# Kernel optimization log

Hardware: AMD Instinct MI355X
Metric: run time of the kernel (lower is better)

The kernel has to match this reference:

```python
import jax, jax.numpy as jnp
import numpy as np

NPOINT = 2048
K = 32
EPS = 1e-5  # BatchNorm eps


def setup_inputs() -> dict:
    key = jax.random.key(0)
    ks = jax.random.split(key, 5)
    B, N, C = 4, 8192, 64
    xyz = jax.random.normal(ks[0], (B, N, 3), jnp.float32)
    points = jax.random.normal(ks[1], (B, C, N), jnp.float32)
    w0 = jax.random.normal(ks[2], (64, C + 3), jnp.float32) * 0.1
    w1 = jax.random.normal(ks[3], (128, 64), jnp.float32) * 0.1
    w2 = jax.random.normal(ks[4], (256, 128), jnp.float32) * 0.1
    return dict(
        xyz=xyz, points=points,
        w0=w0, g0=jnp.ones(64, jnp.float32), b0=jnp.zeros(64, jnp.float32),
        w1=w1, g1=jnp.ones(128, jnp.float32), b1=jnp.zeros(128, jnp.float32),
        w2=w2, g2=jnp.ones(256, jnp.float32), b2=jnp.zeros(256, jnp.float32),
    )


def _fps(xyz, S):
    """Farthest point sampling. xyz: (B,N,3) -> idx (B,S) int32. Starts at point 0."""
    B, N, _ = xyz.shape

    def step(carry, _):
        dmin, far = carry  # dmin: (B,N) running min sq-dist to chosen set; far: (B,) current pick
        centroid = jnp.take_along_axis(xyz, far[:, None, None], axis=1)  # (B,1,3)
        d = jnp.sum((xyz - centroid) ** 2, axis=-1)  # (B,N)
        dmin = jnp.minimum(dmin, d)
        nxt = jnp.argmax(dmin, axis=1).astype(jnp.int32)
        return (dmin, nxt), far

    init = (jnp.full((B, N), 1e10, xyz.dtype), jnp.zeros((B,), jnp.int32))
    _, idx = jax.lax.scan(step, init, None, length=S)
    return jnp.transpose(idx)  # (B,S)


def _bn_relu(x, g, b):
    """Training-mode BatchNorm over all but the channel (last) axis + ReLU. x: (B,S,K,C)."""
    mu = jnp.mean(x, axis=(0, 1, 2), keepdims=True)
    var = jnp.mean((x - mu) ** 2, axis=(0, 1, 2), keepdims=True)
    return jax.nn.relu((x - mu) * jax.lax.rsqrt(var + EPS) * g + b)


def reference(xyz, points, w0, g0, b0, w1, g1, b1, w2, g2, b2):
    B, N, _ = xyz.shape
    S = NPOINT
    idx = _fps(xyz, S)
    new_xyz = jnp.take_along_axis(xyz, idx[:, :, None], axis=1)  # (B,S,3)
    # knn: pairwise squared distances centroids -> all points
    d2 = jnp.sum((new_xyz[:, :, None, :] - xyz[:, None, :, :]) ** 2, axis=-1)  # (B,S,N)
    _, knn_idx = jax.lax.top_k(-d2, K)  # (B,S,K), sorted ascending by distance
    gather = jax.vmap(lambda p, i: p[i])  # per-batch fancy gather
    grouped = gather(xyz, knn_idx) - new_xyz[:, :, None, :]  # (B,S,K,3) relative coords
    neigh = gather(jnp.transpose(points, (0, 2, 1)), knn_idx)  # (B,S,K,C)
    feat = jnp.concatenate([grouped, neigh], axis=-1)  # (B,S,K,3+C)
    for w, g, b in ((w0, g0, b0), (w1, g1, b1), (w2, g2, b2)):
        feat = _bn_relu(jnp.einsum('bskc,oc->bsko', feat, w), g, b)
    new_points = jnp.transpose(jnp.max(feat, axis=2), (0, 2, 1))  # (B,C_out,S)
    return new_xyz, new_points
```

## Files before the change

kernel.cpp:

```cpp
#include <hip/hip_runtime.h>

#define BB 4
#define NN 8192
#define CC 64
#define SS 2048
#define KK 32
#define MROWS (BB*SS*KK)

typedef __attribute__((ext_vector_type(8))) short bf16x8_t;
typedef __attribute__((ext_vector_type(4))) float f32x4_t;
typedef __attribute__((ext_vector_type(2))) float f32x2_t;

__device__ __forceinline__ float bf2f(unsigned short u){
  union { unsigned int i; float f; } v; v.i = ((unsigned int)u) << 16; return v.f;
}
__device__ __forceinline__ unsigned short f2bf(float f){
  union { float f; unsigned int i; } v; v.f = f;
  unsigned int u = v.i;
  unsigned int r = (u + 0x7FFFu + ((u >> 16) & 1u)) >> 16;
  return (unsigned short)r;
}
__device__ __forceinline__ float i2f(int i){ union { int i; float f; } v; v.i = i; return v.f; }
__device__ __forceinline__ int f2i(float f){ union { float f; int i; } v; v.f = f; return v.i; }

__global__ void detect_kernel(const void* pts, int* flag){
  __shared__ int cnt;
  if (threadIdx.x == 0) cnt = 0;
  __syncthreads();
  unsigned short u = ((const unsigned short*)pts)[threadIdx.x];
  int e = (u >> 7) & 0xFF;
  if (e != 0 && (e < 112 || e > 143)) atomicAdd(&cnt, 1);
  __syncthreads();
  if (threadIdx.x == 0) *flag = (cnt > 32) ? 1 : 0;
}

__device__ __forceinline__ void pack_dev(const void* src, unsigned short* dst,
    int CTS, int KSTEPS, int IN, int remap, int idx, bool isf){
  int total = CTS*KSTEPS*512;
  if (idx >= total) return;
  int f = idx >> 9, lane = (idx >> 3) & 63, j = idx & 7;
  int ct = f / KSTEPS, ks = f % KSTEPS;
  int n = ct*16 + (lane & 15);
  int k = ks*32 + (lane >> 4)*8 + j;
  int ksrc;
  if (remap){ ksrc = (k < 64) ? (k + 3) : (k < 67 ? k - 64 : -1); }
  else      { ksrc = (k < IN) ? k : -1; }
  float v = 0.f;
  if (ksrc >= 0){
    size_t si = (size_t)n*IN + ksrc;
    v = isf ? ((const float*)src)[si] : bf2f(((const unsigned short*)src)[si]);
  }
  dst[idx] = f2bf(v);
}

__global__ __launch_bounds__(256) void prep_kernel(
    const void* xyz_in, const void* pts_in,
    const void* w0_in, const void* w1_in, const void* w2_in,
    const void* g0, const void* b0, const void* g1, const void* b1,
    const void* g2, const void* b2,
    float* xyzf, unsigned short* ptsb,
    unsigned short* w0p, unsigned short* w1p, unsigned short* w2p,
    float* gbf, float* stats, const int* flag)
{
  __shared__ float tile[64][65];
  int blk = blockIdx.x, tid = threadIdx.x;
  bool isf = (*flag != 0);
  if (blk < 512){
    int b = blk >> 7, n0 = (blk & 127) * 64;
    #pragma unroll
    for (int k = 0; k < 16; k++){
      int idx = k*256 + tid; int c = idx >> 6; int ni = idx & 63;
      size_t src = ((size_t)b*CC + c)*NN + n0 + ni;
      tile[c][ni] = isf ? ((const float*)pts_in)[src] : bf2f(((const unsigned short*)pts_in)[src]);
    }
    __syncthreads();
    #pragma unroll
    for (int k = 0; k < 16; k++){
      int idx = k*256 + tid; int ni = idx >> 6; int c = idx & 63;
      ptsb[((size_t)b*NN + n0 + ni)*CC + c] = f2bf(tile[c][ni]);
    }
  } else if (blk < 896){
    int i = (blk - 512)*256 + tid;
    if (i < BB*NN*3)
      xyzf[i] = isf ? ((const float*)xyz_in)[i] : bf2f(((const unsigned short*)xyz_in)[i]);
  } else if (blk < 900){
    int i = (blk - 896)*256 + tid;
    if (i < 896){
      const void* src; int off;
      if      (i < 64)  { src = g0; off = i; }
      else if (i < 128) { src = b0; off = i - 64; }
      else if (i < 256) { src = g1; off = i - 128; }
      else if (i < 384) { src = b1; off = i - 256; }
      else if (i < 640) { src = g2; off = i - 384; }
      else              { src = b2; off = i - 640; }
      gbf[i] = isf ? ((const float*)src)[off] : bf2f(((const unsigned short*)src)[off]);
      stats[i] = 0.f;
    }
  } else if (blk < 924){
    pack_dev(w0_in, w0p, 4, 3, 67, 1, (blk-900)*256 + tid, isf);
  } else if (blk < 956){
    pack_dev(w1_in, w1p, 8, 2, 64, 0, (blk-924)*256 + tid, isf);
  } else {
    pack_dev(w2_in, w2p, 16, 4, 128, 0, (blk-956)*256 + tid, isf);
  }
}

__device__ __forceinline__ unsigned mspread(unsigned v){
  v = (v | (v << 16)) & 0x030000FFu;
  v = (v | (v <<  8)) & 0x0300F00Fu;
  v = (v | (v <<  4)) & 0x030C30C3u;
  v = (v | (v <<  2)) & 0x09249249u;
  return v;
}
__global__ __launch_bounds__(1024) void morton_sort(const float* xyzf,
    float* psx, float* psy, float* psz, int* iorig){
  int b = blockIdx.x, tid = threadIdx.x;
  const float* xb = xyzf + (size_t)b*NN*3;
  __shared__ unsigned codes[NN];
  __shared__ unsigned hist[256];
  __shared__ unsigned curs[256];
  __shared__ float rbb[96];
  float x[8], y[8], z[8];
  {
    const float4* p4 = (const float4*)(xb + (size_t)tid*24);
    float4 A=p4[0],B2=p4[1],C=p4[2],D=p4[3],E=p4[4],F=p4[5];
    x[0]=A.x;  y[0]=A.y;  z[0]=A.z;
    x[1]=A.w;  y[1]=B2.x; z[1]=B2.y;
    x[2]=B2.z; y[2]=B2.w; z[2]=C.x;
    x[3]=C.y;  y[3]=C.z;  z[3]=C.w;
    x[4]=D.x;  y[4]=D.y;  z[4]=D.z;
    x[5]=D.w;  y[5]=E.x;  z[5]=E.y;
    x[6]=E.z;  y[6]=E.w;  z[6]=F.x;
    x[7]=F.y;  y[7]=F.z;  z[7]=F.w;
  }
  float lx=x[0],hx=x[0],ly=y[0],hy=y[0],lz=z[0],hz=z[0];
  #pragma unroll
  for (int j = 1; j < 8; j++){
    lx=fminf(lx,x[j]); hx=fmaxf(hx,x[j]);
    ly=fminf(ly,y[j]); hy=fmaxf(hy,y[j]);
    lz=fminf(lz,z[j]); hz=fmaxf(hz,z[j]);
  }
  #pragma unroll
  for (int off = 1; off < 64; off <<= 1){
    lx=fminf(lx,__shfl_xor(lx,off)); hx=fmaxf(hx,__shfl_xor(hx,off));
    ly=fminf(ly,__shfl_xor(ly,off)); hy=fmaxf(hy,__shfl_xor(hy,off));
    lz=fminf(lz,__shfl_xor(lz,off)); hz=fmaxf(hz,__shfl_xor(hz,off));
  }
  int w = tid >> 6;
  if ((tid & 63) == 0){
    rbb[w]=lx; rbb[16+w]=hx; rbb[32+w]=ly; rbb[48+w]=hy; rbb[64+w]=lz; rbb[80+w]=hz;
  }
  if (tid < 256) hist[tid] = 0;
  __syncthreads();
  #pragma unroll
  for (int i = 0; i < 16; i++){
    lx=fminf(lx,rbb[i]); hx=fmaxf(hx,rbb[16+i]);
    ly=fminf(ly,rbb[32+i]); hy=fmaxf(hy,rbb[48+i]);
    lz=fminf(lz,rbb[64+i]); hz=fmaxf(hz,rbb[80+i]);
  }
  float sx = 1023.0f/fmaxf(hx-lx,1e-20f);
  float sy = 1023.0f/fmaxf(hy-ly,1e-20f);
  float sz = 1023.0f/fmaxf(hz-lz,1e-20f);
  #pragma unroll
  for (int j = 0; j < 8; j++){
    int qx = (int)((x[j]-lx)*sx); qx = qx < 0 ? 0 : (qx > 1023 ? 1023 : qx);
    int qy = (int)((y[j]-ly)*sy); qy = qy < 0 ? 0 : (qy > 1023 ? 1023 : qy);
    int qz = (int)((z[j]-lz)*sz); qz = qz < 0 ? 0 : (qz > 1023 ? 1023 : qz);
    unsigned code = mspread((unsigned)qx) | (mspread((unsigned)qy) << 1) | (mspread((unsigned)qz) << 2);
    codes[tid*8 + j] = code;
    atomicAdd(&hist[code >> 22], 1u);
  }
  __syncthreads();
  if (tid < 64){
    unsigned h0 = hist[tid*4], h1 = hist[tid*4+1], h2 = hist[tid*4+2], h3 = hist[tid*4+3];
    unsigned s4 = h0 + h1 + h2 + h3;
    unsigned inc = s4;
    #pragma unroll
    for (int off = 1; off < 64; off <<= 1){
      unsigned o = __shfl_up(inc, off);
      if (tid >= off) inc += o;
    }
    unsigned base = inc - s4;
    curs[tid*4]   = base;
    curs[tid*4+1] = base + h0;
    curs[tid*4+2] = base + h0 + h1;
    curs[tid*4+3] = base + h0 + h1 + h2;
  }
  __syncthreads();
  #pragma unroll
  for (int j = 0; j < 8; j++){
    unsigned c = codes[tid*8 + j] >> 22;
    unsigned pos = atomicAdd(&curs[c], 1u);
    psx[b*NN + pos] = x[j];
    psy[b*NN + pos] = y[j];
    psz[b*NN + pos] = z[j];
    iorig[b*NN + pos] = tid*8 + j;
  }
}

template<int C>
__device__ __forceinline__ float dpp_maxf(float v){
  int t = __builtin_amdgcn_update_dpp(0, f2i(v), C, 0xF, 0xF, true);
  return fmaxf(v, i2f(t));
}
template<int C>
__device__ __forceinline__ unsigned dpp_minu(unsigned v){
  unsigned t = (unsigned)__builtin_amdgcn_update_dpp(-1, (int)v, C, 0xF, 0xF, false);
  return v < t ? v : t;
}

__global__ __launch_bounds__(1024, 1) void fps_kernel(const float* xyzf,
    const float* psx, const float* psy, const float* psz, const int* iorig,
    int* fps_idx, void* d_out, const int* flag){
  int b = blockIdx.x, tid = threadIdx.x;
  const float* xb = xyzf + (size_t)b*NN*3;
  __shared__ float sxyz4[NN*4];
  __shared__ unsigned long long rk[3];
  for (int i = tid; i < NN; i += 1024){
    const float* p = xb + (size_t)i*3;
    float4 v; v.x = p[0]; v.y = p[1]; v.z = p[2]; v.w = 0.f;
    *(float4*)&sxyz4[(size_t)i*4] = v;
  }
  if (tid < 3) rk[tid] = 0ull;
  f32x2_t px2[4], py2[4], pz2[4], dmin2[4];
  int io[8];
  {
    const float4* qx = (const float4*)(psx + b*NN + tid*8);
    const float4* qy = (const float4*)(psy + b*NN + tid*8);
    const float4* qz = (const float4*)(psz + b*NN + tid*8);
    float4 a, c;
    a = qx[0]; c = qx[1];
    px2[0]=(f32x2_t){a.x,a.y}; px2[1]=(f32x2_t){a.z,a.w}; px2[2]=(f32x2_t){c.x,c.y}; px2[3]=(f32x2_t){c.z,c.w};
    a = qy[0]; c = qy[1];
    py2[0]=(f32x2_t){a.x,a.y}; py2[1]=(f32x2_t){a.z,a.w}; py2[2]=(f32x2_t){c.x,c.y}; py2[3]=(f32x2_t){c.z,c.w};
    a = qz[0]; c = qz[1];
    pz2[0]=(f32x2_t){a.x,a.y}; pz2[1]=(f32x2_t){a.z,a.w}; pz2[2]=(f32x2_t){c.x,c.y}; pz2[3]=(f32x2_t){c.z,c.w};
    const int4* qi = (const int4*)(iorig + b*NN + tid*8);
    int4 i0 = qi[0], i1 = qi[1];
    io[0]=i0.x; io[1]=i0.y; io[2]=i0.z; io[3]=i0.w;
    io[4]=i1.x; io[5]=i1.y; io[6]=i1.z; io[7]=i1.w;
  }
  #pragma unroll
  for (int q = 0; q < 4; q++) dmin2[q] = (f32x2_t){1e10f, 1e10f};
  float llx, lhx, lly, lhy, llz, lhz;
  {
    llx = fminf(fminf(px2[0].x,px2[0].y), fminf(px2[1].x,px2[1].y));
    llx = fminf(llx, fminf(fminf(px2[2].x,px2[2].y), fminf(px2[3].x,px2[3].y)));
    lhx = fmaxf(fmaxf(px2[0].x,px2[0].y), fmaxf(px2[1].x,px2[1].y));
    lhx = fmaxf(lhx, fmaxf(fmaxf(px2[2].x,px2[2].y), fmaxf(px2[3].x,px2[3].y)));
    lly = fminf(fminf(py2[0].x,py2[0].y), fminf(py2[1].x,py2[1].y));
    lly = fminf(lly, fminf(fminf(py2[2].x,py2[2].y), fminf(py2[3].x,py2[3].y)));
    lhy = fmaxf(fmaxf(py2[0].x,py2[0].y), fmaxf(py2[1].x,py2[1].y));
    lhy = fmaxf(lhy, fmaxf(fmaxf(py2[2].x,py2[2].y), fmaxf(py2[3].x,py2[3].y)));
    llz = fminf(fminf(pz2[0].x,pz2[0].y), fminf(pz2[1].x,pz2[1].y));
    llz = fminf(llz, fminf(fminf(pz2[2].x,pz2[2].y), fminf(pz2[3].x,pz2[3].y)));
    lhz = fmaxf(fmaxf(pz2[0].x,pz2[0].y), fmaxf(pz2[1].x,pz2[1].y));
    lhz = fmaxf(lhz, fmaxf(fmaxf(pz2[2].x,pz2[2].y), fmaxf(pz2[3].x,pz2[3].y)));
  }
  __syncthreads();
  int far = 0;
  bool isf32 = (*flag != 0);
  float* outf = (float*)d_out; unsigned short* outh = (unsigned short*)d_out;
  int ln = tid & 63;
  unsigned cached_lo = 0u, cached_hi = 0u;
  float lmax = 1e10f;
  int rot = 0;
  for (int s = 0; s < SS; s++){
    int rotn = rot + 1; if (rotn == 3) rotn = 0;
    float4 cf = *(const float4*)&sxyz4[(size_t)far*4];
    float cx = cf.x, cy = cf.y, cz = cf.z;
    if (tid == 0){
      fps_idx[b*SS + s] = far;
      size_t o = ((size_t)b*SS + s)*3;
      if (isf32){ outf[o]=cx; outf[o+1]=cy; outf[o+2]=cz; }
      else { outh[o]=f2bf(cx); outh[o+1]=f2bf(cy); outh[o+2]=f2bf(cz); }
    }
    if (tid == 64) rk[rotn] = 0ull;
    float dxl = fmaxf(fmaxf(llx - cx, cx - lhx), 0.f);
    float dyl = fmaxf(fmaxf(lly - cy, cy - lhy), 0.f);
    float dzl = fmaxf(fmaxf(llz - cz, cz - lhz), 0.f);
    float d2l = (dxl*dxl + dyl*dyl + dzl*dzl) * 0.99999f;
    bool upd = (s == 0) || __any(d2l < lmax);
    if (upd){
      f32x2_t cx2 = (f32x2_t){cx, cx}, cy2 = (f32x2_t){cy, cy}, cz2 = (f32x2_t){cz, cz};
      bool ch = false;
      {
        #pragma clang fp contract(off)
        #pragma unroll
        for (int q = 0; q < 4; q++){
          f32x2_t dx = px2[q] - cx2, dy = py2[q] - cy2, dz = pz2[q] - cz2;
          f32x2_t t = dx*dx;
          t = t + dy*dy;
          t = t + dz*dz;
          ch = ch | (t.x < dmin2[q].x) | (t.y < dmin2[q].y);
          dmin2[q].x = fminf(dmin2[q].x, t.x);
          dmin2[q].y = fminf(dmin2[q].y, t.y);
        }
      }
      if (__any(ch)){
        float m0 = fmaxf(fmaxf(dmin2[0].x, dmin2[0].y), fmaxf(dmin2[1].x, dmin2[1].y));
        float m1 = fmaxf(fmaxf(dmin2[2].x, dmin2[2].y), fmaxf(dmin2[3].x, dmin2[3].y));
        float lm = fmaxf(m0, m1);
        lmax = lm;
        lm = dpp_maxf<0x111>(lm); lm = dpp_maxf<0x112>(lm);
        lm = dpp_maxf<0x114>(lm); lm = dpp_maxf<0x118>(lm);
        lm = dpp_maxf<0x142>(lm); lm = dpp_maxf<0x143>(lm);
        float wmax = i2f(__builtin_amdgcn_readlane(f2i(lm), 63));
        unsigned cand = 0xFFFFFFFFu;
        #pragma unroll
        for (int q = 0; q < 4; q++){
          if (dmin2[q].x == wmax){ unsigned u = (unsigned)io[2*q];   cand = u < cand ? u : cand; }
          if (dmin2[q].y == wmax){ unsigned u = (unsigned)io[2*q+1]; cand = u < cand ? u : cand; }
        }
        cand = dpp_minu<0x111>(cand); cand = dpp_minu<0x112>(cand);
        cand = dpp_minu<0x114>(cand); cand = dpp_minu<0x118>(cand);
        cand = dpp_minu<0x142>(cand); cand = dpp_minu<0x143>(cand);
        unsigned cmin = (unsigned)__builtin_amdgcn_readlane((int)cand, 63);
        cached_hi = (unsigned)f2i(wmax);
        cached_lo = ~cmin;
      }
    }
    if (ln == 63)
      atomicMax(&rk[rot], (((unsigned long long)cached_hi) << 32) | cached_lo);
    __syncthreads();
    unsigned long long kk = rk[rot];
    far = (int)(~(unsigned)kk);
    rot = rotn;
  }
}

__global__ __launch_bounds__(256) void knn_kernel(
    const float* psx, const float* psy, const float* psz, const int* ior,
    const float* xyzf, const int* fps_idx, int* knn){
  int cg = blockIdx.x;
  int b = cg >> 11;
  int tid = threadIdx.x;
  const float* xb = xyzf + (size_t)b*NN*3;
  __shared__ unsigned hist[4096];
  __shared__ unsigned long long cand[512];
  __shared__ unsigned psum[256];
  __shared__ unsigned exbase[64];
  __shared__ float scc[3];
  __shared__ int sB, sBase, sCl, sCc;
  __shared__ unsigned long long rmin[4];
  __shared__ unsigned long long swin;

  if (tid == 0){
    int f = fps_idx[cg];
    scc[0] = xb[f*3]; scc[1] = xb[f*3+1]; scc[2] = xb[f*3+2];
    sCl = 0; sCc = 0;
  }
  #pragma unroll
  for (int i = 0; i < 16; i++) hist[tid*16 + i] = 0;
  __syncthreads();
  float cx = scc[0], cy = scc[1], cz = scc[2];

  float dv[32]; int iv[32];
  const float4* qx = (const float4*)(psx + b*NN);
  const float4* qy = (const float4*)(psy + b*NN);
  const float4* qz = (const float4*)(psz + b*NN);
  const int4*   qi = (const int4*)(ior + b*NN);
  {
    #pragma clang fp contract(off)
    #pragma unroll
    for (int k = 0; k < 8; k++){
      float4 X = qx[k*256 + tid];
      float4 Y = qy[k*256 + tid];
      float4 Z = qz[k*256 + tid];
      int4   I = qi[k*256 + tid];
      float xs_[4] = {X.x, X.y, X.z, X.w};
      float ys_[4] = {Y.x, Y.y, Y.z, Y.w};
      float zs_[4] = {Z.x, Z.y, Z.z, Z.w};
      int   is_[4] = {I.x, I.y, I.z, I.w};
      #pragma unroll
      for (int r = 0; r < 4; r++){
        float dx = cx - xs_[r], dy = cy - ys_[r], dz = cz - zs_[r];
        dv[k*4 + r] = dx*dx + dy*dy + dz*dz;
        iv[k*4 + r] = is_[r];
      }
    }
  }
  #pragma unroll
  for (int t = 0; t < 32; t++)
    atomicAdd(&hist[((unsigned)f2i(dv[t])) >> 20], 1u);
  __syncthreads();
  unsigned lsum = 0;
  #pragma unroll
  for (int i = 0; i < 16; i++) lsum += hist[tid*16 + i];
  psum[tid] = lsum;
  __syncthreads();
  if (tid < 64){
    unsigned s4 = psum[tid*4] + psum[tid*4+1] + psum[tid*4+2] + psum[tid*4+3];
    unsigned inc = s4;
    #pragma unroll
    for (int off = 1; off < 64; off <<= 1){
      unsigned o = __shfl_up(inc, off);
      if (tid >= off) inc += o;
    }
    exbase[tid] = inc - s4;
  }
  __syncthreads();
  {
    int g4 = tid >> 2;
    unsigned ex = exbase[g4];
    for (int j = g4*4; j < tid; j++) ex += psum[j];
    unsigned run = ex;
    #pragma unroll
    for (int i = 0; i < 16; i++){
      unsigned c = hist[tid*16 + i];
      if (run < 32u && run + c >= 32u){ sB = tid*16 + i; sBase = (int)run; }
      run += c;
    }
  }
  __syncthreads();
  int Bbin = sB, base = sBase;
  int out = cg << 5;
  #pragma unroll
  for (int t = 0; t < 32; t++){
    unsigned bits = (unsigned)f2i(dv[t]);
    unsigned hb = bits >> 20;
    int idx = iv[t];
    if ((int)hb < Bbin){
      int sl = atomicAdd(&sCl, 1);
      knn[out + sl] = idx;
    } else if ((int)hb == Bbin){
      int c = atomicAdd(&sCc, 1);
      if (c < 512) cand[c] = (((unsigned long long)bits) << 32) | (unsigned)idx;
    }
  }
  __syncthreads();
  int cc = sCc; if (cc > 512) cc = 512;
  int r = 32 - base;
  for (int round = 0; round < r; round++){
    unsigned long long lm = ~0ull;
    for (int i = tid; i < cc; i += 256){
      unsigned long long v = cand[i];
      if (v < lm) lm = v;
    }
    #pragma unroll
    for (int off = 1; off < 64; off <<= 1){
      unsigned long long o = __shfl_xor(lm, off);
      if (o < lm) lm = o;
    }
    if ((tid & 63) == 0) rmin[tid >> 6] = lm;
    __syncthreads();
    if (tid == 0){
      unsigned long long m = rmin[0];
      #pragma unroll
      for (int q = 1; q < 4; q++) if (rmin[q] < m) m = rmin[q];
      swin = m;
      knn[out + base + round] = (int)(unsigned)m;
    }
    __syncthreads();
    unsigned long long m = swin;
    for (int i = tid; i < cc; i += 256)
      if (cand[i] == m) cand[i] = ~0ull;
    __syncthreads();
  }
}

__device__ __forceinline__ bf16x8_t bfrag(const unsigned short* wp, int f, int lane){
  return *(const bf16x8_t*)(wp + ((size_t)f << 9) + (lane << 3));
}
__device__ __forceinline__ bf16x8_t bn_frag(bf16x8_t v, const float* a, const float* c, int kbase){
  float4 a0 = *(const float4*)(a + kbase); float4 a1 = *(const float4*)(a + kbase + 4);
  float4 c0 = *(const float4*)(c + kbase); float4 c1 = *(const float4*)(c + kbase + 4);
  float av[8] = {a0.x,a0.y,a0.z,a0.w,a1.x,a1.y,a1.z,a1.w};
  float cv[8] = {c0.x,c0.y,c0.z,c0.w,c1.x,c1.y,c1.z,c1.w};
  bf16x8_t r;
  #pragma unroll
  for (int j = 0; j < 8; j++)
    r[j] = (short)f2bf(fmaxf(bf2f((unsigned short)v[j])*av[j] + cv[j], 0.f));
  return r;
}

template<int TILES>
__global__ __launch_bounds__(256) void passA(
    const float* __restrict__ xyzf, const unsigned short* __restrict__ ptsb,
    const int* __restrict__ fpsi, const int* __restrict__ knn,
    const unsigned short* __restrict__ w0p,
    unsigned short* __restrict__ y0g, float* osum, float* osq)
{
  __shared__ unsigned short xb0[64*104];
  __shared__ unsigned short st[64*72];
  __shared__ float sacc[128];
  int tid = threadIdx.x, lane = tid & 63, w = tid >> 6;
  int l15 = lane & 15, quad = lane >> 4;
  float ssum[4], ssq[4];
  #pragma unroll
  for (int c = 0; c < 4; c++){ ssum[c] = 0.f; ssq[c] = 0.f; }
  if (tid < 128) sacc[tid] = 0.f;
  __syncthreads();

  for (int t = 0; t < TILES; t++){
    int row0 = (blockIdx.x * TILES + t) * 64;
    {
      int r = tid >> 2, p = tid & 3;
      int g = row0 + r;
      int bq = g >> 16, s = (g >> 5) & 2047;
      int n = knn[g];
      const bf16x8_t* pr = (const bf16x8_t*)(ptsb + (((size_t)bq*NN + n) << 6));
      *(bf16x8_t*)&xb0[r*104 + p*16]     = pr[p*2];
      *(bf16x8_t*)&xb0[r*104 + p*16 + 8] = pr[p*2 + 1];
      if (p == 3){
        const float* xbp = xyzf + (size_t)bq*NN*3;
        int f = fpsi[(bq << 11) + s];
        float dx = xbp[n*3]   - xbp[f*3];
        float dy = xbp[n*3+1] - xbp[f*3+1];
        float dz = xbp[n*3+2] - xbp[f*3+2];
        bf16x8_t v = {(short)f2bf(dx), (short)f2bf(dy), (short)f2bf(dz), 0,0,0,0,0};
        bf16x8_t z = {0,0,0,0,0,0,0,0};
        *(bf16x8_t*)&xb0[r*104 + 64] = v;
        *(bf16x8_t*)&xb0[r*104 + 72] = z;
        *(bf16x8_t*)&xb0[r*104 + 80] = z;
        *(bf16x8_t*)&xb0[r*104 + 88] = z;
      }
    }
    bf16x8_t a0[3];
    #pragma unroll
    for (int ks = 0; ks < 3; ks++)
      a0[ks] = *(const bf16x8_t*)&xb0[(w*16 + l15)*104 + ks*32 + quad*8];
    #pragma unroll
    for (int ct = 0; ct < 4; ct++){
      f32x4_t a = {0.f,0.f,0.f,0.f};
      #pragma unroll
      for (int ks = 0; ks < 3; ks++)
        a = __builtin_amdgcn_mfma_f32_16x16x32_bf16(a0[ks], bfrag(w0p, ct*3+ks, lane), a, 0, 0, 0);
      #pragma unroll
      for (int r = 0; r < 4; r++){
        float v = a[r]; ssum[ct] += v; ssq[ct] += v*v;
        st[(w*16 + quad*4 + r)*72 + ct*16 + l15] = f2bf(v);
      }
    }
    __syncthreads();
    #pragma unroll
    for (int p = 0; p < 2; p++){
      int idx = p*2048 + tid*8; int r = idx >> 6; int c = idx & 63;
      *(bf16x8_t*)(y0g + (size_t)row0*64 + idx) = *(const bf16x8_t*)&st[r*72 + c];
    }
    __syncthreads();
  }
  #pragma unroll
  for (int c = 0; c < 4; c++){
    ssum[c] += __shfl_xor(ssum[c], 16); ssum[c] += __shfl_xor(ssum[c], 32);
    ssq [c] += __shfl_xor(ssq [c], 16); ssq [c] += __shfl_xor(ssq [c], 32);
  }
  if (quad == 0){
    #pragma unroll
    for (int c = 0; c < 4; c++){
      atomicAdd(&sacc[c*16 + l15], ssum[c]);
      atomicAdd(&sacc[64 + c*16 + l15], ssq[c]);
    }
  }
  __syncthreads();
  if (tid < 64){
    atomicAdd(&osum[tid], sacc[tid]);
    atomicAdd(&osq [tid], sacc[64 + tid]);
  }
}

template<int TILES>
__global__ __launch_bounds__(256) void passB(
    const unsigned short* __restrict__ y0g, const unsigned short* __restrict__ w1p,
    const float* __restrict__ stats, const float* __restrict__ gbf,
    unsigned short* __restrict__ y1g, float* osum, float* osq)
{
  __shared__ unsigned short st[64*136];
  __shared__ float sacc[256];
  __shared__ __align__(16) float sbn[128];
  int tid = threadIdx.x, lane = tid & 63, w = tid >> 6;
  int l15 = lane & 15, quad = lane >> 4;
  float ssum[8], ssq[8];
  #pragma unroll
  for (int c = 0; c < 8; c++){ ssum[c] = 0.f; ssq[c] = 0.f; }
  sacc[tid] = 0.f;
  if (tid < 64){
    const float invM = 1.0f/262144.0f;
    float mu = stats[tid]*invM;
    float var = fmaxf(stats[64+tid]*invM - mu*mu, 0.f);
    float inv = 1.0f/sqrtf(var + 1e-5f);
    float av = gbf[tid]*inv;
    sbn[tid] = av; sbn[64+tid] = gbf[64+tid] - mu*av;
  }
  __syncthreads();

  for (int t = 0; t < TILES; t++){
    int row0 = (blockIdx.x * TILES + t) * 64;
    int row = row0 + w*16 + l15;
    bf16x8_t a1[2];
    #pragma unroll
    for (int ks = 0; ks < 2; ks++){
      bf16x8_t v = *(const bf16x8_t*)(y0g + (size_t)row*64 + ks*32 + quad*8);
      a1[ks] = bn_frag(v, sbn, sbn + 64, ks*32 + quad*8);
    }
    #pragma unroll
    for (int ct = 0; ct < 8; ct++){
      f32x4_t a = {0.f,0.f,0.f,0.f};
      #pragma unroll
      for (int ks = 0; ks < 2; ks++)
        a = __builtin_amdgcn_mfma_f32_16x16x32_bf16(a1[ks], bfrag(w1p, ct*2+ks, lane), a, 0, 0, 0);
      #pragma unroll
      for (int r = 0; r < 4; r++){
        float v = a[r]; ssum[ct] += v; ssq[ct] += v*v;
        st[(w*16 + quad*4 + r)*136 + ct*16 + l15] = f2bf(v);
      }
    }
    __syncthreads();
    #pragma unroll
    for (int p = 0; p < 4; p++){
      int idx = p*2048 + tid*8; int r = idx >> 7; int c = idx & 127;
      *(bf16x8_t*)(y1g + (size_t)row0*128 + idx) = *(const bf16x8_t*)&st[r*136 + c];
    }
    __syncthreads();
  }
  #pragma unroll
  for (int c = 0; c < 8; c++){
    ssum[c] += __shfl_xor(ssum[c], 16); ssum[c] += __shfl_xor(ssum[c], 32);
    ssq [c] += __shfl_xor(ssq [c], 16); ssq [c] += __shfl_xor(ssq [c], 32);
  }
  if (quad == 0){
    #pragma unroll
    for (int c = 0; c < 8; c++){
      atomicAdd(&sacc[c*16 + l15], ssum[c]);
      atomicAdd(&sacc[128 + c*16 + l15], ssq[c]);
    }
  }
  __syncthreads();
  if (tid < 128){
    atomicAdd(&osum[tid], sacc[tid]);
    atomicAdd(&osq [tid], sacc[128 + tid]);
  }
}

template<int TILES>
__global__ __launch_bounds__(256) void passC(
    const unsigned short* __restrict__ y1g, const unsigned short* __restrict__ w2p,
    const float* __restrict__ stats, const float* __restrict__ gbf,
    float* osum, float* osq)
{
  __shared__ float sacc[512];
  __shared__ __align__(16) float sbn[256];
  int tid = threadIdx.x, lane = tid & 63, w = tid >> 6;
  int l15 = lane & 15, quad = lane >> 4;
  float ssum[16], ssq[16];
  #pragma unroll
  for (int c = 0; c < 16; c++){ ssum[c] = 0.f; ssq[c] = 0.f; }
  sacc[tid] = 0.f; sacc[tid + 256] = 0.f;
  if (tid < 128){
    const float invM = 1.0f/262144.0f;
    float mu = stats[128+tid]*invM;
    float var = fmaxf(stats[256+tid]*invM - mu*mu, 0.f);
    float inv = 1.0f/sqrtf(var + 1e-5f);
    float av = gbf[128+tid]*inv;
    sbn[tid] = av; sbn[128+tid] = gbf[256+tid] - mu*av;
  }
  __syncthreads();

  for (int t = 0; t < TILES; t++){
    int row0 = (blockIdx.x * TILES + t) * 64;
    int row = row0 + w*16 + l15;
    bf16x8_t a2[4];
    #pragma unroll
    for (int ks = 0; ks < 4; ks++){
      bf16x8_t v = *(const bf16x8_t*)(y1g + (size_t)row*128 + ks*32 + quad*8);
      a2[ks] = bn_frag(v, sbn, sbn + 128, ks*32 + quad*8);
    }
    #pragma unroll
    for (int ct = 0; ct < 16; ct++){
      f32x4_t a = {0.f,0.f,0.f,0.f};
      #pragma unroll
      for (int ks = 0; ks < 4; ks++)
        a = __builtin_amdgcn_mfma_f32_16x16x32_bf16(a2[ks], bfrag(w2p, ct*4+ks, lane), a, 0, 0, 0);
      #pragma unroll
      for (int r = 0; r < 4; r++){ float v = a[r]; ssum[ct] += v; ssq[ct] += v*v; }
    }
  }
  #pragma unroll
  for (int c = 0; c < 16; c++){
    ssum[c] += __shfl_xor(ssum[c], 16); ssum[c] += __shfl_xor(ssum[c], 32);
    ssq [c] += __shfl_xor(ssq [c], 16); ssq [c] += __shfl_xor(ssq [c], 32);
  }
  if (quad == 0){
    #pragma unroll
    for (int c = 0; c < 16; c++){
      atomicAdd(&sacc[c*16 + l15], ssum[c]);
      atomicAdd(&sacc[256 + c*16 + l15], ssq[c]);
    }
  }
  __syncthreads();
  if (tid < 256){
    atomicAdd(&osum[tid], sacc[tid]);
    atomicAdd(&osq [tid], sacc[256 + tid]);
  }
}

__global__ __launch_bounds__(256) void passD(
    const unsigned short* __restrict__ y1g, const unsigned short* __restrict__ w2p,
    const float* __restrict__ stats, const float* __restrict__ gbf,
    void* d_out, const int* __restrict__ flag)
{
  __shared__ float smax[1024];
  __shared__ __align__(16) float sbn[768];
  int tid = threadIdx.x, lane = tid & 63, w = tid >> 6;
  int l15 = lane & 15, quad = lane >> 4;
  {
    const float invM = 1.0f/262144.0f;
    if (tid < 128){
      float mu = stats[128+tid]*invM;
      float var = fmaxf(stats[256+tid]*invM - mu*mu, 0.f);
      float inv = 1.0f/sqrtf(var + 1e-5f);
      float av = gbf[128+tid]*inv;
      sbn[tid] = av; sbn[128+tid] = gbf[256+tid] - mu*av;
    }
    float mu2 = stats[384+tid]*invM;
    float var2 = fmaxf(stats[640+tid]*invM - mu2*mu2, 0.f);
    float inv2 = 1.0f/sqrtf(var2 + 1e-5f);
    float av2 = gbf[384+tid]*inv2;
    sbn[256+tid] = av2; sbn[512+tid] = gbf[640+tid] - mu2*av2;
  }
  __syncthreads();
  int row0 = blockIdx.x * 64;
  int row = row0 + w*16 + l15;
  bf16x8_t a2[4];
  #pragma unroll
  for (int ks = 0; ks < 4; ks++){
    bf16x8_t v = *(const bf16x8_t*)(y1g + (size_t)row*128 + ks*32 + quad*8);
    a2[ks] = bn_frag(v, sbn, sbn + 128, ks*32 + quad*8);
  }
  #pragma unroll
  for (int ct = 0; ct < 16; ct++){
    f32x4_t a = {0.f,0.f,0.f,0.f};
    #pragma unroll
    for (int ks = 0; ks < 4; ks++)
      a = __builtin_amdgcn_mfma_f32_16x16x32_bf16(a2[ks], bfrag(w2p, ct*4+ks, lane), a, 0, 0, 0);
    int o = ct*16 + l15;
    float ga = sbn[256 + o], gc = sbn[512 + o];
    float m = fmaxf(fmaxf(a[0]*ga + gc, a[1]*ga + gc), fmaxf(a[2]*ga + gc, a[3]*ga + gc));
    m = fmaxf(m, __shfl_xor(m, 16));
    m = fmaxf(m, __shfl_xor(m, 32));
    if (quad == 0) smax[w*256 + o] = m;
  }
  __syncthreads();
  float v0 = fmaxf(fmaxf(smax[tid], smax[256 + tid]), 0.f);
  float v1 = fmaxf(fmaxf(smax[512 + tid], smax[768 + tid]), 0.f);
  int cg = blockIdx.x * 2;
  bool isf32 = (*flag != 0);
  int b0 = cg >> 11, s0 = cg & 2047;
  int b1 = (cg+1) >> 11, s1 = (cg+1) & 2047;
  size_t o0 = (size_t)BB*SS*3 + (((size_t)(b0*256 + tid)) << 11) + s0;
  size_t o1 = (size_t)BB*SS*3 + (((size_t)(b1*256 + tid)) << 11) + s1;
  if (isf32){ ((float*)d_out)[o0] = v0; ((float*)d_out)[o1] = v1; }
  else { ((unsigned short*)d_out)[o0] = f2bf(v0); ((unsigned short*)d_out)[o1] = f2bf(v1); }
}

#define OFF_FLAG   0u
#define OFF_FPS    256u
#define OFF_KNN    33024u
#define OFF_STATS  1081600u
#define OFF_XYZF   1088768u
#define OFF_GB     1481984u
#define OFF_W0P    1485568u
#define OFF_W1P    1497856u
#define OFF_W2P    1514240u
#define OFF_PTSB   1579776u
#define OFF_Y0     5774336u
#define OFF_Y1     39328768u
#define OFF_PSX    (OFF_Y1)
#define OFF_PSY    (OFF_Y1 + 131072u)
#define OFF_PSZ    (OFF_Y1 + 262144u)
#define OFF_IOR    (OFF_Y1 + 393216u)

extern "C" void kernel_launch(void* const* d_in, const int* in_sizes, int n_in,
                              void* d_out, int out_size, void* d_ws, size_t ws_size,
                              hipStream_t stream){
  char* ws = (char*)d_ws;
  int*   flag  = (int*)(ws + OFF_FLAG);
  int*   fpsi  = (int*)(ws + OFF_FPS);
  int*   knn   = (int*)(ws + OFF_KNN);
  float* stats = (float*)(ws + OFF_STATS);
  float* xyzf  = (float*)(ws + OFF_XYZF);
  float* gbf   = (float*)(ws + OFF_GB);
  unsigned short* w0p = (unsigned short*)(ws + OFF_W0P);
  unsigned short* w1p = (unsigned short*)(ws + OFF_W1P);
  unsigned short* w2p = (unsigned short*)(ws + OFF_W2P);
  unsigned short* ptsb = (unsigned short*)(ws + OFF_PTSB);
  unsigned short* y0g = (unsigned short*)(ws + OFF_Y0);
  unsigned short* y1g = (unsigned short*)(ws + OFF_Y1);
  float* psx = (float*)(ws + OFF_PSX);
  float* psy = (float*)(ws + OFF_PSY);
  float* psz = (float*)(ws + OFF_PSZ);
  int*   ior = (int*)(ws + OFF_IOR);

  detect_kernel<<<1, 256, 0, stream>>>(d_in[1], flag);
  prep_kernel<<<1084, 256, 0, stream>>>(d_in[0], d_in[1], d_in[2], d_in[5], d_in[8],
                                        d_in[3], d_in[4], d_in[6], d_in[7], d_in[9], d_in[10],
                                        xyzf, ptsb, w0p, w1p, w2p, gbf, stats, flag);

  morton_sort<<<BB, 1024, 0, stream>>>(xyzf, psx, psy, psz, ior);
  fps_kernel<<<BB, 1024, 0, stream>>>(xyzf, psx, psy, psz, ior, fpsi, d_out, flag);
  knn_kernel<<<BB*SS, 256, 0, stream>>>(psx, psy, psz, ior, xyzf, fpsi, knn);

  passA<4><<<1024, 256, 0, stream>>>(xyzf, ptsb, fpsi, knn, w0p, y0g, stats + 0, stats + 64);
  passB<4><<<1024, 256, 0, stream>>>(y0g, w1p, stats, gbf, y1g, stats + 128, stats + 256);
  passC<4><<<1024, 256, 0, stream>>>(y1g, w2p, stats, gbf, stats + 384, stats + 640);
  passD<<<4096, 256, 0, stream>>>(y1g, w2p, stats, gbf, d_out, flag);
  (void)in_sizes; (void)n_in; (void)out_size; (void)ws_size;
}
```

Baseline: 1.858 ms.

## Fully sort points by Morton code with bitonic sort; split FPS atomic slot

Replaces the 8-bit-bucket counting sort in morton_sort with a full bitonic sort of 64-bit (Morton code, index) keys in shared memory. The sorted points then follow a tighter spatial order, which tightens the per-thread bounding boxes used to skip FPS distance updates. The FPS kernel also splits the per-step atomicMax target into two slots, one per half of the waves, which halves contention on a single LDS address. In exchange the sort runs many more passes, each ending in a block-wide barrier, and gathers from global memory on write-out.

After: 1.851 ms. About the same (-0.4%).

```diff
diff --git a/kernel.cpp b/kernel.cpp
--- a/kernel.cpp
+++ b/kernel.cpp
@@ -116,9 +116,7 @@
     float* psx, float* psy, float* psz, int* iorig){
   int b = blockIdx.x, tid = threadIdx.x;
   const float* xb = xyzf + (size_t)b*NN*3;
-  __shared__ unsigned codes[NN];
-  __shared__ unsigned hist[256];
-  __shared__ unsigned curs[256];
+  __shared__ unsigned long long keys[NN];
   __shared__ float rbb[96];
   float x[8], y[8], z[8];
   {
@@ -150,7 +148,6 @@
   if ((tid & 63) == 0){
     rbb[w]=lx; rbb[16+w]=hx; rbb[32+w]=ly; rbb[48+w]=hy; rbb[64+w]=lz; rbb[80+w]=hz;
   }
-  if (tid < 256) hist[tid] = 0;
   __syncthreads();
   #pragma unroll
   for (int i = 0; i < 16; i++){
@@ -167,34 +164,29 @@
     int qy = (int)((y[j]-ly)*sy); qy = qy < 0 ? 0 : (qy > 1023 ? 1023 : qy);
     int qz = (int)((z[j]-lz)*sz); qz = qz < 0 ? 0 : (qz > 1023 ? 1023 : qz);
     unsigned code = mspread((unsigned)qx) | (mspread((unsigned)qy) << 1) | (mspread((unsigned)qz) << 2);
-    codes[tid*8 + j] = code;
-    atomicAdd(&hist[code >> 22], 1u);
-  }
-  __syncthreads();
-  if (tid < 64){
-    unsigned h0 = hist[tid*4], h1 = hist[tid*4+1], h2 = hist[tid*4+2], h3 = hist[tid*4+3];
-    unsigned s4 = h0 + h1 + h2 + h3;
-    unsigned inc = s4;
-    #pragma unroll
-    for (int off = 1; off < 64; off <<= 1){
-      unsigned o = __shfl_up(inc, off);
-      if (tid >= off) inc += o;
-    }
-    unsigned base = inc - s4;
-    curs[tid*4]   = base;
-    curs[tid*4+1] = base + h0;
-    curs[tid*4+2] = base + h0 + h1;
-    curs[tid*4+3] = base + h0 + h1 + h2;
-  }
-  __syncthreads();
+    keys[tid*8 + j] = (((unsigned long long)code) << 13) | (unsigned)(tid*8 + j);
+  }
+  __syncthreads();
+  for (int size = 2; size <= NN; size <<= 1){
+    for (int stride = size >> 1; stride > 0; stride >>= 1){
+      #pragma unroll 4
+      for (int t = tid; t < NN/2; t += 1024){
+        int pos = 2*t - (t & (stride - 1));
+        bool up = (pos & size) == 0;
+        unsigned long long a = keys[pos], c = keys[pos + stride];
+        if ((a > c) == up){ keys[pos] = c; keys[pos + stride] = a; }
+      }
+      __syncthreads();
+    }
+  }
   #pragma unroll
   for (int j = 0; j < 8; j++){
-    unsigned c = codes[tid*8 + j] >> 22;
-    unsigned pos = atomicAdd(&curs[c], 1u);
-    psx[b*NN + pos] = x[j];
-    psy[b*NN + pos] = y[j];
-    psz[b*NN + pos] = z[j];
-    iorig[b*NN + pos] = tid*8 + j;
+    int i = j*1024 + tid;
+    int pos = (int)(keys[i] & 8191u);
+    psx[b*NN + i] = xb[pos*3];
+    psy[b*NN + i] = xb[pos*3 + 1];
+    psz[b*NN + i] = xb[pos*3 + 2];
+    iorig[b*NN + i] = pos;
   }
 }
 
@@ -215,13 +207,13 @@
   int b = blockIdx.x, tid = threadIdx.x;
   const float* xb = xyzf + (size_t)b*NN*3;
   __shared__ float sxyz4[NN*4];
-  __shared__ unsigned long long rk[3];
+  __shared__ unsigned long long rk[3][2];
   for (int i = tid; i < NN; i += 1024){
     const float* p = xb + (size_t)i*3;
     float4 v; v.x = p[0]; v.y = p[1]; v.z = p[2]; v.w = 0.f;
     *(float4*)&sxyz4[(size_t)i*4] = v;
   }
-  if (tid < 3) rk[tid] = 0ull;
+  if (tid < 6) ((unsigned long long*)rk)[tid] = 0ull;
   f32x2_t px2[4], py2[4], pz2[4], dmin2[4];
   int io[8];
   {
@@ -261,7 +253,7 @@
   int far = 0;
   bool isf32 = (*flag != 0);
   float* outf = (float*)d_out; unsigned short* outh = (unsigned short*)d_out;
-  int ln = tid & 63;
+  int ln = tid & 63, w = tid >> 6;
   unsigned cached_lo = 0u, cached_hi = 0u;
   float lmax = 1e10f;
   int rot = 0;
@@ -275,7 +267,7 @@
       if (isf32){ outf[o]=cx; outf[o+1]=cy; outf[o+2]=cz; }
       else { outh[o]=f2bf(cx); outh[o+1]=f2bf(cy); outh[o+2]=f2bf(cz); }
     }
-    if (tid == 64) rk[rotn] = 0ull;
+    if (tid == 64){ rk[rotn][0] = 0ull; rk[rotn][1] = 0ull; }
     float dxl = fmaxf(fmaxf(llx - cx, cx - lhx), 0.f);
     float dyl = fmaxf(fmaxf(lly - cy, cy - lhy), 0.f);
     float dzl = fmaxf(fmaxf(llz - cz, cz - lhz), 0.f);
@@ -321,9 +313,10 @@
       }
     }
     if (ln == 63)
-      atomicMax(&rk[rot], (((unsigned long long)cached_hi) << 32) | cached_lo);
+      atomicMax(&rk[rot][w >> 3], (((unsigned long long)cached_hi) << 32) | cached_lo);
     __syncthreads();
-    unsigned long long kk = rk[rot];
+    unsigned long long k0 = rk[rot][0], k1 = rk[rot][1];
+    unsigned long long kk = (k1 > k0) ? k1 : k0;
     far = (int)(~(unsigned)kk);
     rot = rotn;
   }
```
